# Optimization experiments

Hardware: AMD Instinct MI355X
Metric: run time of the kernel (lower is better)

## Reference

```python
import jax, jax.numpy as jnp
import numpy as np

B, T, I, H, L = 256, 256, 16, 512, 4


def _lstm_layer(x, w_ih, w_hh, b_ih, b_hh):
    """One PyTorch-style LSTM layer. x: [B,T,Din] -> [B,T,H]. Gate order i,f,g,o."""
    Bn = x.shape[0]
    Hn = w_hh.shape[1]
    # precompute input contribution for all timesteps (both biases folded in)
    xg = jnp.einsum('btd,gd->btg', x, w_ih) + b_ih + b_hh  # [B,T,4H]

    def step(carry, xg_t):
        h, c = carry
        g = xg_t + h @ w_hh.T  # [B,4H]
        i, f, gg, o = jnp.split(g, 4, axis=-1)
        i = jax.nn.sigmoid(i)
        f = jax.nn.sigmoid(f)
        gg = jnp.tanh(gg)
        o = jax.nn.sigmoid(o)
        c = f * c + i * gg
        h = o * jnp.tanh(c)
        return (h, c), h

    init = (jnp.zeros((Bn, Hn), x.dtype), jnp.zeros((Bn, Hn), x.dtype))
    _, hs = jax.lax.scan(step, init, jnp.swapaxes(xg, 0, 1))  # hs: [T,B,H]
    return jnp.swapaxes(hs, 0, 1)


def setup_inputs() -> dict:
    key = jax.random.key(0)
    ks = jax.random.split(key, 12)
    s = 1.0 / np.sqrt(H)  # PyTorch LSTM init scale
    inp = {
        'x': jax.random.normal(ks[0], (B, T, I), jnp.float32),
        'w_ih0': jax.random.normal(ks[1], (4 * H, I), jnp.float32) * s,
        'w_hh0': jax.random.normal(ks[2], (4 * H, H), jnp.float32) * s,
        'b_ih0': jax.random.normal(ks[3], (4 * H,), jnp.float32) * s,
        'b_hh0': jax.random.normal(ks[4], (4 * H,), jnp.float32) * s,
        'w_ih_r': jax.random.normal(ks[5], (L - 1, 4 * H, H), jnp.float32) * s,
        'w_hh_r': jax.random.normal(ks[6], (L - 1, 4 * H, H), jnp.float32) * s,
        'b_ih_r': jax.random.normal(ks[7], (L - 1, 4 * H), jnp.float32) * s,
        'b_hh_r': jax.random.normal(ks[8], (L - 1, 4 * H), jnp.float32) * s,
        'fc_w': jax.random.normal(ks[9], (1, H), jnp.float32) * s,
        'fc_b': jax.random.normal(ks[10], (1,), jnp.float32) * s,
    }
    return inp


def reference(x, w_ih0, w_hh0, b_ih0, b_hh0, w_ih_r, w_hh_r, b_ih_r, b_hh_r, fc_w, fc_b):
    # 4-layer LSTM (eval mode: inter-layer dropout is identity)
    h = _lstm_layer(x, w_ih0, w_hh0, b_ih0, b_hh0)
    for l in range(L - 1):
        h = _lstm_layer(h, w_ih_r[l], w_hh_r[l], b_ih_r[l], b_hh_r[l])
    last = h[:, -1, :]  # [B,H]
    return jax.nn.sigmoid(last @ fc_w.T + fc_b)  # [B,1]
```

## Files before the change

kernel.cpp:

```cpp
#include <hip/hip_runtime.h>

#define BB 256
#define TT 256
#define II 16
#define HH 512
#define G4 2048
#define LL 4

typedef float f32x4 __attribute__((ext_vector_type(4)));
typedef _Float16 f16x8 __attribute__((ext_vector_type(8)));
typedef _Float16 f16x4 __attribute__((ext_vector_type(4)));
typedef float f32x4v __attribute__((ext_vector_type(4)));
typedef unsigned int u32x4 __attribute__((ext_vector_type(4)));

#define MFMA16(a, b, c) __builtin_amdgcn_mfma_f32_16x16x32_f16((a), (b), (c), 0, 0, 0)

__device__ _Float16 g_hbuf[(size_t)LL * BB * TT * HH];
__device__ _Float16 g_xbf[(size_t)BB * TT * II];
__device__ _Float16 g_wih0[G4 * II];
__device__ _Float16 g_whh[(size_t)LL * G4 * HH];
__device__ _Float16 g_wihr[(size_t)3 * G4 * HH];
__device__ float    g_bias[LL * G4];
__device__ unsigned g_cnt[32 * 64];

__device__ __forceinline__ void st_cv(void* p, unsigned v) {
  asm volatile("global_store_dword %0, %1, off sc0 sc1" : : "v"(p), "v"(v) : "memory");
}
__device__ __forceinline__ float fsig(float x) { return 1.f / (1.f + __expf(-x)); }
__device__ __forceinline__ float ftanh(float x) { return 1.f - 2.f / (__expf(2.f * x) + 1.f); }

__device__ __forceinline__ unsigned ld_ctr(const unsigned* p) {
  return __hip_atomic_load(p, __ATOMIC_RELAXED, __HIP_MEMORY_SCOPE_AGENT);
}

__device__ __forceinline__ f16x8 ldsA(const _Float16* base, int mt, int kt, int lane) {
  int row = mt * 16 + (lane & 15);
  int off = (row << 10) + (kt << 6) + ((lane >> 4) << 4);
  off ^= (lane & 15) << 4;
  return *(const f16x8*)((const char*)base + off);
}

__device__ __forceinline__ void cv4(_Float16* d, const float* s, size_t n4, size_t tid, size_t stride) {
  for (size_t i = tid; i < n4; i += stride) {
    f32x4v v = ((const f32x4v*)s)[i];
    ((f16x4*)d)[i] = __builtin_convertvector(v, f16x4);
  }
}

__global__ void prep_kernel(const float* __restrict__ x, const float* __restrict__ wih0,
                            const float* __restrict__ whh0, const float* __restrict__ bih0,
                            const float* __restrict__ bhh0, const float* __restrict__ wihr,
                            const float* __restrict__ whhr, const float* __restrict__ bihr,
                            const float* __restrict__ bhhr) {
  size_t tid = (size_t)blockIdx.x * blockDim.x + threadIdx.x;
  size_t stride = (size_t)gridDim.x * blockDim.x;
  cv4(g_xbf, x, (size_t)BB * TT * II / 4, tid, stride);
  cv4(g_wih0, wih0, (size_t)G4 * II / 4, tid, stride);
  cv4(g_whh, whh0, (size_t)G4 * HH / 4, tid, stride);
  cv4(g_whh + (size_t)G4 * HH, whhr, (size_t)3 * G4 * HH / 4, tid, stride);
  cv4(g_wihr, wihr, (size_t)3 * G4 * HH / 4, tid, stride);
  for (size_t i = tid; i < G4; i += stride) g_bias[i] = bih0[i] + bhh0[i];
  for (size_t i = tid; i < 3 * G4; i += stride) g_bias[G4 + i] = bihr[i] + bhhr[i];
  if (tid < 32) g_cnt[tid * 64] = 0u;
}

__global__ __launch_bounds__(256, 1) void lstm_kernel() {
  const int tid = threadIdx.x;
  const int g = blockIdx.x & 7;
  const int jc = blockIdx.x >> 3;
  const int w = tid >> 6;
  const int lane = tid & 63;
  const int col = lane & 15, kg = lane >> 4;
  const int n0 = w * 512 + jc * 16;

  __shared__ _Float16 xs[32 * 512];
  __shared__ _Float16 hs[32 * 512];
  __shared__ float gbuf[4][32 * 17];

  const int eb = tid >> 3;
  const int ej = (tid & 7) * 2;

  f16x8 wihf[16], whhf[16];
  unsigned* cown = &g_cnt[g * 64];

  if (tid < 64) {
    int row = tid >> 1, half = tid & 1;
    int off = (row << 10) + 32 + (half << 4); off ^= (row & 15) << 4;
    u32x4 z = {0u, 0u, 0u, 0u};
    *(u32x4*)((char*)xs + off) = z;
  }

  for (int l = 0; l < LL; ++l) {
    {
      const _Float16* wb = g_whh + ((size_t)l * G4 + (n0 + col)) * HH + kg * 8;
#pragma unroll
      for (int kt = 0; kt < 16; ++kt) whhf[kt] = *(const f16x8*)(wb + kt * 32);
      if (l == 0) {
        if (kg < 2) wihf[0] = *(const f16x8*)(g_wih0 + (n0 + col) * II + kg * 8);
        else { f16x8 z = {}; wihf[0] = z; }
      } else {
        const _Float16* wi = g_wihr + ((size_t)(l - 1) * G4 + (n0 + col)) * HH + kg * 8;
#pragma unroll
        for (int kt = 0; kt < 16; ++kt) wihf[kt] = *(const f16x8*)(wi + kt * 32);
      }
    }
    const float bias = g_bias[l * G4 + n0 + col];
    float c0 = 0.f, c1 = 0.f;

    const _Float16* xsrc = g_hbuf + ((size_t)(l - 1) * BB + 32 * g) * TT * HH;
    _Float16* hdst = g_hbuf + ((size_t)l * BB + 32 * g) * TT * HH;

    u32x4 vx[8], vx0;
    if (l > 0) {
#pragma unroll
      for (int it = 0; it < 8; ++it) {
        int q = tid + it * 256, row = q >> 6, c16 = q & 63;
        vx[it] = *(const u32x4*)((const char*)(xsrc + (size_t)row * TT * HH) + c16 * 16);
      }
    } else if (tid < 64) {
      int row = tid >> 1, half = tid & 1;
      vx0 = *(const u32x4*)(g_xbf + ((size_t)(32 * g + row) * TT) * II + half * 8);
    }

    for (int t = 0; t < TT; ++t) {
      if (l > 0) {
#pragma unroll
        for (int it = 0; it < 8; ++it) {
          int q = tid + it * 256, row = q >> 6, c16 = q & 63;
          int off = (row << 10) + (c16 << 4); off ^= (row & 15) << 4;
          *(u32x4*)((char*)xs + off) = vx[it];
        }
      } else if (tid < 64) {
        int row = tid >> 1, half = tid & 1;
        int off = (row << 10) + (half << 4); off ^= (row & 15) << 4;
        *(u32x4*)((char*)xs + off) = vx0;
      }

      if (t > 0 && tid == 0) {
        unsigned tgt = 32u * (unsigned)(l * TT + t);
        while (ld_ctr(cown) < tgt) {}
      }
      __syncthreads();

      u32x4 vh[8];
      if (t > 0) {
        const _Float16* sh = hdst + (size_t)(t - 1) * HH;
#pragma unroll
        for (int it = 0; it < 8; ++it) {
          int q = tid + it * 256, row = q >> 6, c16 = q & 63;
          vh[it] = *(const u32x4*)((const char*)(sh + (size_t)row * TT * HH) + c16 * 16);
        }
      }

      f32x4 acc0 = {bias, bias, bias, bias}, acc1 = acc0;
      if (l == 0) {
        acc0 = MFMA16(ldsA(xs, 0, 0, lane), wihf[0], acc0);
        acc1 = MFMA16(ldsA(xs, 1, 0, lane), wihf[0], acc1);
      } else {
#pragma unroll
        for (int kt = 0; kt < 16; ++kt) {
          acc0 = MFMA16(ldsA(xs, 0, kt, lane), wihf[kt], acc0);
          acc1 = MFMA16(ldsA(xs, 1, kt, lane), wihf[kt], acc1);
        }
      }

      if (t > 0) {
#pragma unroll
        for (int it = 0; it < 8; ++it) {
          int q = tid + it * 256, row = q >> 6, c16 = q & 63;
          int off = (row << 10) + (c16 << 4); off ^= (row & 15) << 4;
          *(u32x4*)((char*)hs + off) = vh[it];
        }
        __syncthreads();
      }
      if (t + 1 < TT) {
        if (l > 0) {
          const _Float16* sx = xsrc + (size_t)(t + 1) * HH;
#pragma unroll
          for (int it = 0; it < 8; ++it) {
            int q = tid + it * 256, row = q >> 6, c16 = q & 63;
            vx[it] = *(const u32x4*)((const char*)(sx + (size_t)row * TT * HH) + c16 * 16);
          }
        } else if (tid < 64) {
          int row = tid >> 1, half = tid & 1;
          vx0 = *(const u32x4*)(g_xbf + ((size_t)(32 * g + row) * TT + (t + 1)) * II + half * 8);
        }
      }
      if (t > 0) {
#pragma unroll
        for (int kt = 0; kt < 16; ++kt) {
          acc0 = MFMA16(ldsA(hs, 0, kt, lane), whhf[kt], acc0);
          acc1 = MFMA16(ldsA(hs, 1, kt, lane), whhf[kt], acc1);
        }
      }

#pragma unroll
      for (int r = 0; r < 4; ++r) {
        gbuf[w][(kg * 4 + r) * 17 + col] = acc0[r];
        gbuf[w][(16 + kg * 4 + r) * 17 + col] = acc1[r];
      }
      __syncthreads();

      {
        int i0 = eb * 17 + ej;
        float i_0 = fsig(gbuf[0][i0]),  i_1 = fsig(gbuf[0][i0 + 1]);
        float f_0 = fsig(gbuf[1][i0]),  f_1 = fsig(gbuf[1][i0 + 1]);
        float t_0 = ftanh(gbuf[2][i0]), t_1 = ftanh(gbuf[2][i0 + 1]);
        float o_0 = fsig(gbuf[3][i0]),  o_1 = fsig(gbuf[3][i0 + 1]);
        c0 = f_0 * c0 + i_0 * t_0;
        c1 = f_1 * c1 + i_1 * t_1;
        float h0 = o_0 * ftanh(c0), h1 = o_1 * ftanh(c1);
        _Float16 hh0 = (_Float16)h0, hh1 = (_Float16)h1;
        unsigned pv = ((unsigned)__builtin_bit_cast(unsigned short, hh1) << 16) |
                      (unsigned)__builtin_bit_cast(unsigned short, hh0);
        _Float16* dst = hdst + ((size_t)eb * TT + t) * HH + jc * 16 + ej;
        st_cv(dst, pv);
      }

      asm volatile("s_waitcnt vmcnt(0)" ::: "memory");
      __syncthreads();
      if (tid == 0) {
        __hip_atomic_fetch_add(cown, 1u, __ATOMIC_RELAXED, __HIP_MEMORY_SCOPE_AGENT);
      }
    }
  }
}

__global__ void fc_kernel(const float* __restrict__ fcw, const float* __restrict__ fcb,
                          float* __restrict__ out) {
  int b = blockIdx.x, lane = threadIdx.x;
  const _Float16* h = g_hbuf + ((size_t)3 * BB + b) * TT * HH + (size_t)(TT - 1) * HH + lane * 8;
  f16x8 hv = *(const f16x8*)h;
  const float* wp = fcw + lane * 8;
  float s = 0.f;
#pragma unroll
  for (int j = 0; j < 8; ++j) s += (float)hv[j] * wp[j];
#pragma unroll
  for (int off = 32; off; off >>= 1) s += __shfl_down(s, off, 64);
  if (lane == 0) out[b] = 1.f / (1.f + __expf(-(s + fcb[0])));
}

extern "C" void kernel_launch(void* const* d_in, const int* in_sizes, int n_in,
                              void* d_out, int out_size, void* d_ws, size_t ws_size,
                              hipStream_t stream) {
  const float* x    = (const float*)d_in[0];
  const float* wih0 = (const float*)d_in[1];
  const float* whh0 = (const float*)d_in[2];
  const float* bih0 = (const float*)d_in[3];
  const float* bhh0 = (const float*)d_in[4];
  const float* wihr = (const float*)d_in[5];
  const float* whhr = (const float*)d_in[6];
  const float* bihr = (const float*)d_in[7];
  const float* bhhr = (const float*)d_in[8];
  const float* fcw  = (const float*)d_in[9];
  const float* fcb  = (const float*)d_in[10];

  prep_kernel<<<dim3(1024), dim3(256), 0, stream>>>(x, wih0, whh0, bih0, bhh0,
                                                    wihr, whhr, bihr, bhhr);
  lstm_kernel<<<dim3(256), dim3(256), 0, stream>>>();
  fc_kernel<<<dim3(256), dim3(64), 0, stream>>>(fcw, fcb, (float*)d_out);
}
```

Before: 4.994 ms.

## Interleave two batch groups per block with per-producer flags and tiled h layout

Halves the grid to 128 blocks, each processing two batch groups in alternation so one group's sync wait can overlap the other's compute. Replaces the shared atomic counter per group with per-producer flag words polled by 32 threads. Changes the hidden-state buffer to a tiled [layer][group][t][jc][row][16] layout so that each block writes a contiguous 1KB chunk with dwordx4 stores and reads contiguous 16KB blobs. The cost is serialized work for two groups per block on fewer CUs, plus more barriers.

```diff
diff --git a/kernel.cpp b/kernel.cpp
--- a/kernel.cpp
+++ b/kernel.cpp
@@ -15,23 +15,28 @@
 
 #define MFMA16(a, b, c) __builtin_amdgcn_mfma_f32_16x16x32_f16((a), (b), (c), 0, 0, 0)
 
-__device__ _Float16 g_hbuf[(size_t)LL * BB * TT * HH];
+__device__ _Float16 g_hx[(size_t)LL * 8 * TT * 32 * 32 * 16];
 __device__ _Float16 g_xbf[(size_t)BB * TT * II];
 __device__ _Float16 g_wih0[G4 * II];
 __device__ _Float16 g_whh[(size_t)LL * G4 * HH];
 __device__ _Float16 g_wihr[(size_t)3 * G4 * HH];
 __device__ float    g_bias[LL * G4];
-__device__ unsigned g_cnt[32 * 64];
-
-__device__ __forceinline__ void st_cv(void* p, unsigned v) {
+__device__ unsigned g_flag[256 * 16];
+
+__device__ __forceinline__ unsigned ld_cv32(const unsigned* p) {
+  unsigned r;
+  asm volatile("global_load_dword %0, %1, off sc0 sc1\n\ts_waitcnt vmcnt(0)"
+               : "=v"(r) : "v"(p) : "memory");
+  return r;
+}
+__device__ __forceinline__ void st_cv32(unsigned* p, unsigned v) {
   asm volatile("global_store_dword %0, %1, off sc0 sc1" : : "v"(p), "v"(v) : "memory");
+}
+__device__ __forceinline__ void st_cv16(void* p, u32x4 v) {
+  asm volatile("global_store_dwordx4 %0, %1, off sc0 sc1" : : "v"(p), "v"(v) : "memory");
 }
 __device__ __forceinline__ float fsig(float x) { return 1.f / (1.f + __expf(-x)); }
 __device__ __forceinline__ float ftanh(float x) { return 1.f - 2.f / (__expf(2.f * x) + 1.f); }
-
-__device__ __forceinline__ unsigned ld_ctr(const unsigned* p) {
-  return __hip_atomic_load(p, __ATOMIC_RELAXED, __HIP_MEMORY_SCOPE_AGENT);
-}
 
 __device__ __forceinline__ f16x8 ldsA(const _Float16* base, int mt, int kt, int lane) {
   int row = mt * 16 + (lane & 15);
@@ -61,13 +66,13 @@
   cv4(g_wihr, wihr, (size_t)3 * G4 * HH / 4, tid, stride);
   for (size_t i = tid; i < G4; i += stride) g_bias[i] = bih0[i] + bhh0[i];
   for (size_t i = tid; i < 3 * G4; i += stride) g_bias[G4 + i] = bihr[i] + bhhr[i];
-  if (tid < 32) g_cnt[tid * 64] = 0u;
+  for (size_t i = tid; i < 256; i += stride) st_cv32(&g_flag[i * 16], 0u);
 }
 
 __global__ __launch_bounds__(256, 1) void lstm_kernel() {
   const int tid = threadIdx.x;
-  const int g = blockIdx.x & 7;
-  const int jc = blockIdx.x >> 3;
+  const int jc = blockIdx.x >> 2;
+  const int gA = blockIdx.x & 3;
   const int w = tid >> 6;
   const int lane = tid & 63;
   const int col = lane & 15, kg = lane >> 4;
@@ -76,18 +81,28 @@
   __shared__ _Float16 xs[32 * 512];
   __shared__ _Float16 hs[32 * 512];
   __shared__ float gbuf[4][32 * 17];
+  __shared__ unsigned hout[32][8];
 
   const int eb = tid >> 3;
-  const int ej = (tid & 7) * 2;
+  const int ej2 = tid & 7;
 
   f16x8 wihf[16], whhf[16];
-  unsigned* cown = &g_cnt[g * 64];
+  u32x4 vx[2][8], vx0[2];
+  float c0[2], c1[2];
+  const int gArr[2] = {gA, gA + 4};
 
   if (tid < 64) {
-    int row = tid >> 1, half = tid & 1;
-    int off = (row << 10) + 32 + (half << 4); off ^= (row & 15) << 4;
+    int row = tid >> 1, part = tid & 1;
+    int off = (row << 10) + 32 + (part << 4); off ^= (row & 15) << 4;
     u32x4 z = {0u, 0u, 0u, 0u};
     *(u32x4*)((char*)xs + off) = z;
+  }
+#pragma unroll
+  for (int sg = 0; sg < 2; ++sg) {
+    if (tid < 64) {
+      int row = tid >> 1, part = tid & 1;
+      vx0[sg] = *(const u32x4*)(g_xbf + ((size_t)(32 * gArr[sg] + row) * TT) * II + part * 8);
+    }
   }
 
   for (int l = 0; l < LL; ++l) {
@@ -105,122 +120,119 @@
       }
     }
     const float bias = g_bias[l * G4 + n0 + col];
-    float c0 = 0.f, c1 = 0.f;
-
-    const _Float16* xsrc = g_hbuf + ((size_t)(l - 1) * BB + 32 * g) * TT * HH;
-    _Float16* hdst = g_hbuf + ((size_t)l * BB + 32 * g) * TT * HH;
-
-    u32x4 vx[8], vx0;
-    if (l > 0) {
-#pragma unroll
-      for (int it = 0; it < 8; ++it) {
-        int q = tid + it * 256, row = q >> 6, c16 = q & 63;
-        vx[it] = *(const u32x4*)((const char*)(xsrc + (size_t)row * TT * HH) + c16 * 16);
-      }
-    } else if (tid < 64) {
-      int row = tid >> 1, half = tid & 1;
-      vx0 = *(const u32x4*)(g_xbf + ((size_t)(32 * g + row) * TT) * II + half * 8);
-    }
+#pragma unroll
+    for (int sg = 0; sg < 2; ++sg) { c0[sg] = 0.f; c1[sg] = 0.f; }
 
     for (int t = 0; t < TT; ++t) {
-      if (l > 0) {
-#pragma unroll
-        for (int it = 0; it < 8; ++it) {
-          int q = tid + it * 256, row = q >> 6, c16 = q & 63;
-          int off = (row << 10) + (c16 << 4); off ^= (row & 15) << 4;
-          *(u32x4*)((char*)xs + off) = vx[it];
-        }
-      } else if (tid < 64) {
-        int row = tid >> 1, half = tid & 1;
-        int off = (row << 10) + (half << 4); off ^= (row & 15) << 4;
-        *(u32x4*)((char*)xs + off) = vx0;
-      }
-
-      if (t > 0 && tid == 0) {
-        unsigned tgt = 32u * (unsigned)(l * TT + t);
-        while (ld_ctr(cown) < tgt) {}
-      }
-      __syncthreads();
-
-      u32x4 vh[8];
-      if (t > 0) {
-        const _Float16* sh = hdst + (size_t)(t - 1) * HH;
-#pragma unroll
-        for (int it = 0; it < 8; ++it) {
-          int q = tid + it * 256, row = q >> 6, c16 = q & 63;
-          vh[it] = *(const u32x4*)((const char*)(sh + (size_t)row * TT * HH) + c16 * 16);
-        }
-      }
-
-      f32x4 acc0 = {bias, bias, bias, bias}, acc1 = acc0;
-      if (l == 0) {
-        acc0 = MFMA16(ldsA(xs, 0, 0, lane), wihf[0], acc0);
-        acc1 = MFMA16(ldsA(xs, 1, 0, lane), wihf[0], acc1);
-      } else {
-#pragma unroll
-        for (int kt = 0; kt < 16; ++kt) {
-          acc0 = MFMA16(ldsA(xs, 0, kt, lane), wihf[kt], acc0);
-          acc1 = MFMA16(ldsA(xs, 1, kt, lane), wihf[kt], acc1);
-        }
-      }
-
-      if (t > 0) {
-#pragma unroll
-        for (int it = 0; it < 8; ++it) {
-          int q = tid + it * 256, row = q >> 6, c16 = q & 63;
-          int off = (row << 10) + (c16 << 4); off ^= (row & 15) << 4;
-          *(u32x4*)((char*)hs + off) = vh[it];
-        }
-        __syncthreads();
-      }
-      if (t + 1 < TT) {
+#pragma unroll
+      for (int sg = 0; sg < 2; ++sg) {
+        const int g = gArr[sg];
+        const size_t blobL = ((size_t)l * 8 + g) * TT;
+
+        const unsigned tgt = (unsigned)(l * TT + t);
+        if (tgt && tid < 64) {
+          const unsigned* fp = &g_flag[(g * 32 + (tid & 31)) * 16];
+          while (ld_cv32(fp) < tgt) {}
+        }
+        __syncthreads();
+
+        if (t == 0 && l > 0) {
+          const char* xb = (const char*)(g_hx + (((size_t)(l - 1) * 8 + g) * TT) * 16384);
+#pragma unroll
+          for (int it = 0; it < 8; ++it)
+            vx[sg][it] = *(const u32x4*)(xb + tid * 16 + it * 4096);
+        }
+        u32x4 vh[8];
+        if (t > 0) {
+          const char* hb = (const char*)(g_hx + (blobL + (t - 1)) * 16384);
+#pragma unroll
+          for (int it = 0; it < 8; ++it)
+            vh[it] = *(const u32x4*)(hb + tid * 16 + it * 4096);
+        }
         if (l > 0) {
-          const _Float16* sx = xsrc + (size_t)(t + 1) * HH;
 #pragma unroll
           for (int it = 0; it < 8; ++it) {
-            int q = tid + it * 256, row = q >> 6, c16 = q & 63;
-            vx[it] = *(const u32x4*)((const char*)(sx + (size_t)row * TT * HH) + c16 * 16);
+            int jcs = (tid >> 6) + it * 4, row = (tid >> 1) & 31, p = tid & 1;
+            int off = (row << 10) + jcs * 32 + (p << 4); off ^= (row & 15) << 4;
+            *(u32x4*)((char*)xs + off) = vx[sg][it];
           }
         } else if (tid < 64) {
-          int row = tid >> 1, half = tid & 1;
-          vx0 = *(const u32x4*)(g_xbf + ((size_t)(32 * g + row) * TT + (t + 1)) * II + half * 8);
-        }
-      }
-      if (t > 0) {
-#pragma unroll
-        for (int kt = 0; kt < 16; ++kt) {
-          acc0 = MFMA16(ldsA(hs, 0, kt, lane), whhf[kt], acc0);
-          acc1 = MFMA16(ldsA(hs, 1, kt, lane), whhf[kt], acc1);
-        }
-      }
-
-#pragma unroll
-      for (int r = 0; r < 4; ++r) {
-        gbuf[w][(kg * 4 + r) * 17 + col] = acc0[r];
-        gbuf[w][(16 + kg * 4 + r) * 17 + col] = acc1[r];
-      }
-      __syncthreads();
-
-      {
-        int i0 = eb * 17 + ej;
-        float i_0 = fsig(gbuf[0][i0]),  i_1 = fsig(gbuf[0][i0 + 1]);
-        float f_0 = fsig(gbuf[1][i0]),  f_1 = fsig(gbuf[1][i0 + 1]);
-        float t_0 = ftanh(gbuf[2][i0]), t_1 = ftanh(gbuf[2][i0 + 1]);
-        float o_0 = fsig(gbuf[3][i0]),  o_1 = fsig(gbuf[3][i0 + 1]);
-        c0 = f_0 * c0 + i_0 * t_0;
-        c1 = f_1 * c1 + i_1 * t_1;
-        float h0 = o_0 * ftanh(c0), h1 = o_1 * ftanh(c1);
-        _Float16 hh0 = (_Float16)h0, hh1 = (_Float16)h1;
-        unsigned pv = ((unsigned)__builtin_bit_cast(unsigned short, hh1) << 16) |
-                      (unsigned)__builtin_bit_cast(unsigned short, hh0);
-        _Float16* dst = hdst + ((size_t)eb * TT + t) * HH + jc * 16 + ej;
-        st_cv(dst, pv);
-      }
-
-      asm volatile("s_waitcnt vmcnt(0)" ::: "memory");
-      __syncthreads();
-      if (tid == 0) {
-        __hip_atomic_fetch_add(cown, 1u, __ATOMIC_RELAXED, __HIP_MEMORY_SCOPE_AGENT);
+          int row = tid >> 1, part = tid & 1;
+          int off = (row << 10) + (part << 4); off ^= (row & 15) << 4;
+          *(u32x4*)((char*)xs + off) = vx0[sg];
+        }
+        __syncthreads();
+
+        f32x4 a0 = {bias, bias, bias, bias}, a1 = a0;
+        if (l == 0) {
+          a0 = MFMA16(ldsA(xs, 0, 0, lane), wihf[0], a0);
+          a1 = MFMA16(ldsA(xs, 1, 0, lane), wihf[0], a1);
+        } else {
+#pragma unroll
+          for (int kt = 0; kt < 16; ++kt) {
+            a0 = MFMA16(ldsA(xs, 0, kt, lane), wihf[kt], a0);
+            a1 = MFMA16(ldsA(xs, 1, kt, lane), wihf[kt], a1);
+          }
+        }
+
+        if (t > 0) {
+#pragma unroll
+          for (int it = 0; it < 8; ++it) {
+            int jcs = (tid >> 6) + it * 4, row = (tid >> 1) & 31, p = tid & 1;
+            int off = (row << 10) + jcs * 32 + (p << 4); off ^= (row & 15) << 4;
+            *(u32x4*)((char*)hs + off) = vh[it];
+          }
+          __syncthreads();
+        }
+        if (t + 1 < TT) {
+          if (l > 0) {
+            const char* xb = (const char*)(g_hx + (((size_t)(l - 1) * 8 + g) * TT + (t + 1)) * 16384);
+#pragma unroll
+            for (int it = 0; it < 8; ++it)
+              vx[sg][it] = *(const u32x4*)(xb + tid * 16 + it * 4096);
+          } else if (tid < 64) {
+            int row = tid >> 1, part = tid & 1;
+            vx0[sg] = *(const u32x4*)(g_xbf + ((size_t)(32 * g + row) * TT + (t + 1)) * II + part * 8);
+          }
+        }
+        if (t > 0) {
+#pragma unroll
+          for (int kt = 0; kt < 16; ++kt) {
+            a0 = MFMA16(ldsA(hs, 0, kt, lane), whhf[kt], a0);
+            a1 = MFMA16(ldsA(hs, 1, kt, lane), whhf[kt], a1);
+          }
+        }
+
+#pragma unroll
+        for (int r = 0; r < 4; ++r) {
+          gbuf[w][(kg * 4 + r) * 17 + col] = a0[r];
+          gbuf[w][(16 + kg * 4 + r) * 17 + col] = a1[r];
+        }
+        __syncthreads();
+
+        {
+          int i0 = eb * 17 + ej2 * 2;
+          float i_0 = fsig(gbuf[0][i0]),  i_1 = fsig(gbuf[0][i0 + 1]);
+          float f_0 = fsig(gbuf[1][i0]),  f_1 = fsig(gbuf[1][i0 + 1]);
+          float t_0 = ftanh(gbuf[2][i0]), t_1 = ftanh(gbuf[2][i0 + 1]);
+          float o_0 = fsig(gbuf[3][i0]),  o_1 = fsig(gbuf[3][i0 + 1]);
+          c0[sg] = f_0 * c0[sg] + i_0 * t_0;
+          c1[sg] = f_1 * c1[sg] + i_1 * t_1;
+          float h0 = o_0 * ftanh(c0[sg]), h1 = o_1 * ftanh(c1[sg]);
+          _Float16 hh0 = (_Float16)h0, hh1 = (_Float16)h1;
+          hout[eb][ej2] = ((unsigned)__builtin_bit_cast(unsigned short, hh1) << 16) |
+                          (unsigned)__builtin_bit_cast(unsigned short, hh0);
+        }
+        __syncthreads();
+
+        if (tid < 64) {
+          int row = tid >> 1, part = tid & 1;
+          u32x4 v = *(const u32x4*)&hout[row][part * 4];
+          _Float16* dst = g_hx + ((blobL + t) * 32 + jc) * 512 + row * 16 + part * 8;
+          st_cv16(dst, v);
+          asm volatile("s_waitcnt vmcnt(0)" ::: "memory");
+          if (tid == 0) st_cv32(&g_flag[(g * 32 + jc) * 16], (unsigned)(l * TT + t + 1));
+        }
       }
     }
   }
@@ -229,7 +241,9 @@
 __global__ void fc_kernel(const float* __restrict__ fcw, const float* __restrict__ fcb,
                           float* __restrict__ out) {
   int b = blockIdx.x, lane = threadIdx.x;
-  const _Float16* h = g_hbuf + ((size_t)3 * BB + b) * TT * HH + (size_t)(TT - 1) * HH + lane * 8;
+  int g = b >> 5, row = b & 31;
+  int jcs = lane >> 1, part = lane & 1;
+  const _Float16* h = g_hx + ((((size_t)3 * 8 + g) * TT + (TT - 1)) * 32 + jcs) * 512 + row * 16 + part * 8;
   f16x8 hv = *(const f16x8*)h;
   const float* wp = fcw + lane * 8;
   float s = 0.f;
@@ -257,6 +271,6 @@
 
   prep_kernel<<<dim3(1024), dim3(256), 0, stream>>>(x, wih0, whh0, bih0, bhh0,
                                                     wihr, whhr, bihr, bhhr);
-  lstm_kernel<<<dim3(256), dim3(256), 0, stream>>>();
+  lstm_kernel<<<dim3(128), dim3(256), 0, stream>>>();
   fc_kernel<<<dim3(256), dim3(64), 0, stream>>>(fcw, fcb, (float*)d_out);
 }
```

After: 8.175 ms. +63.7%, slower.

## Replace counter barrier with poison-sentinel polling on hidden-state data

Applied to the files above, without the earlier changes.

Drops the per-group atomic counter and its spin-wait, along with the end-of-step vmcnt wait, syncthreads and atomic increment. Instead the prep kernel fills the hidden-state buffer with an all-ones poison pattern, and consumers re-load (cache-bypassing) until no poison word remains. The goal is to remove a full round-trip of barrier signalling per timestep so data arrival itself is the synchronisation. In exchange every launch must poison the whole hidden buffer. It also relies on 0xFFFF never being a real fp16 output (it is a NaN pattern) and on the ordering of the 4-byte stores.

```diff
diff --git a/kernel.cpp b/kernel.cpp
--- a/kernel.cpp
+++ b/kernel.cpp
@@ -6,6 +6,7 @@
 #define HH 512
 #define G4 2048
 #define LL 4
+#define POISON 0xFFFFFFFFu
 
 typedef float f32x4 __attribute__((ext_vector_type(4)));
 typedef _Float16 f16x8 __attribute__((ext_vector_type(8)));
@@ -21,16 +22,29 @@
 __device__ _Float16 g_whh[(size_t)LL * G4 * HH];
 __device__ _Float16 g_wihr[(size_t)3 * G4 * HH];
 __device__ float    g_bias[LL * G4];
-__device__ unsigned g_cnt[32 * 64];
-
+
+__device__ __forceinline__ u32x4 ld_cv(const void* p) {
+  u32x4 r;
+  asm volatile("global_load_dwordx4 %0, %1, off sc0 sc1" : "=v"(r) : "v"(p) : "memory");
+  return r;
+}
+__device__ __forceinline__ u32x4 ld_nc(const void* p) {
+  u32x4 r;
+  asm volatile("global_load_dwordx4 %0, %1, off" : "=v"(r) : "v"(p) : "memory");
+  return r;
+}
 __device__ __forceinline__ void st_cv(void* p, unsigned v) {
   asm volatile("global_store_dword %0, %1, off sc0 sc1" : : "v"(p), "v"(v) : "memory");
 }
+#define WAITV0() asm volatile("s_waitcnt vmcnt(0)" ::: "memory")
+#define WAITV1() asm volatile("s_waitcnt vmcnt(1)" ::: "memory")
+
 __device__ __forceinline__ float fsig(float x) { return 1.f / (1.f + __expf(-x)); }
 __device__ __forceinline__ float ftanh(float x) { return 1.f - 2.f / (__expf(2.f * x) + 1.f); }
-
-__device__ __forceinline__ unsigned ld_ctr(const unsigned* p) {
-  return __hip_atomic_load(p, __ATOMIC_RELAXED, __HIP_MEMORY_SCOPE_AGENT);
+__device__ __forceinline__ unsigned max4u(u32x4 v) {
+  unsigned a = v[0] > v[1] ? v[0] : v[1];
+  unsigned b = v[2] > v[3] ? v[2] : v[3];
+  return a > b ? a : b;
 }
 
 __device__ __forceinline__ f16x8 ldsA(const _Float16* base, int mt, int kt, int lane) {
@@ -61,7 +75,10 @@
   cv4(g_wihr, wihr, (size_t)3 * G4 * HH / 4, tid, stride);
   for (size_t i = tid; i < G4; i += stride) g_bias[i] = bih0[i] + bhh0[i];
   for (size_t i = tid; i < 3 * G4; i += stride) g_bias[G4 + i] = bihr[i] + bhhr[i];
-  if (tid < 32) g_cnt[tid * 64] = 0u;
+  u32x4 P = {POISON, POISON, POISON, POISON};
+  size_t n16 = (size_t)LL * BB * TT * HH * 2 / 16;
+  u32x4* hb = (u32x4*)g_hbuf;
+  for (size_t i = tid; i < n16; i += stride) hb[i] = P;
 }
 
 __global__ __launch_bounds__(256, 1) void lstm_kernel() {
@@ -81,7 +98,6 @@
   const int ej = (tid & 7) * 2;
 
   f16x8 wihf[16], whhf[16];
-  unsigned* cown = &g_cnt[g * 64];
 
   if (tid < 64) {
     int row = tid >> 1, half = tid & 1;
@@ -115,15 +131,28 @@
 #pragma unroll
       for (int it = 0; it < 8; ++it) {
         int q = tid + it * 256, row = q >> 6, c16 = q & 63;
-        vx[it] = *(const u32x4*)((const char*)(xsrc + (size_t)row * TT * HH) + c16 * 16);
+        vx[it] = ld_nc((const char*)(xsrc + (size_t)row * TT * HH) + c16 * 16);
       }
     } else if (tid < 64) {
       int row = tid >> 1, half = tid & 1;
-      vx0 = *(const u32x4*)(g_xbf + ((size_t)(32 * g + row) * TT) * II + half * 8);
+      vx0 = ld_nc(g_xbf + ((size_t)(32 * g + row) * TT) * II + half * 8);
     }
 
     for (int t = 0; t < TT; ++t) {
+      if (t == 0) WAITV0(); else WAITV1();
       if (l > 0) {
+        while (true) {
+          unsigned mx = 0u;
+#pragma unroll
+          for (int it = 0; it < 8; ++it) { unsigned m = max4u(vx[it]); mx = mx > m ? mx : m; }
+          if (!__any((int)(mx == POISON))) break;
+#pragma unroll
+          for (int it = 0; it < 8; ++it) {
+            int q = tid + it * 256, row = q >> 6, c16 = q & 63;
+            vx[it] = ld_cv((const char*)(xsrc + (size_t)t * HH + (size_t)row * TT * HH) + c16 * 16);
+          }
+          WAITV0();
+        }
 #pragma unroll
         for (int it = 0; it < 8; ++it) {
           int q = tid + it * 256, row = q >> 6, c16 = q & 63;
@@ -136,35 +165,44 @@
         *(u32x4*)((char*)xs + off) = vx0;
       }
 
-      if (t > 0 && tid == 0) {
-        unsigned tgt = 32u * (unsigned)(l * TT + t);
-        while (ld_ctr(cown) < tgt) {}
-      }
-      __syncthreads();
-
       u32x4 vh[8];
       if (t > 0) {
         const _Float16* sh = hdst + (size_t)(t - 1) * HH;
 #pragma unroll
         for (int it = 0; it < 8; ++it) {
           int q = tid + it * 256, row = q >> 6, c16 = q & 63;
-          vh[it] = *(const u32x4*)((const char*)(sh + (size_t)row * TT * HH) + c16 * 16);
-        }
-      }
-
-      f32x4 acc0 = {bias, bias, bias, bias}, acc1 = acc0;
+          vh[it] = ld_cv((const char*)(sh + (size_t)row * TT * HH) + c16 * 16);
+        }
+      }
+      __syncthreads();
+
+      f32x4 a0 = {bias, bias, bias, bias}, a1 = a0;
       if (l == 0) {
-        acc0 = MFMA16(ldsA(xs, 0, 0, lane), wihf[0], acc0);
-        acc1 = MFMA16(ldsA(xs, 1, 0, lane), wihf[0], acc1);
+        a0 = MFMA16(ldsA(xs, 0, 0, lane), wihf[0], a0);
+        a1 = MFMA16(ldsA(xs, 1, 0, lane), wihf[0], a1);
       } else {
 #pragma unroll
         for (int kt = 0; kt < 16; ++kt) {
-          acc0 = MFMA16(ldsA(xs, 0, kt, lane), wihf[kt], acc0);
-          acc1 = MFMA16(ldsA(xs, 1, kt, lane), wihf[kt], acc1);
+          a0 = MFMA16(ldsA(xs, 0, kt, lane), wihf[kt], a0);
+          a1 = MFMA16(ldsA(xs, 1, kt, lane), wihf[kt], a1);
         }
       }
 
       if (t > 0) {
+        WAITV0();
+        while (true) {
+          unsigned mx = 0u;
+#pragma unroll
+          for (int it = 0; it < 8; ++it) { unsigned m = max4u(vh[it]); mx = mx > m ? mx : m; }
+          if (!__any((int)(mx == POISON))) break;
+          const _Float16* sh = hdst + (size_t)(t - 1) * HH;
+#pragma unroll
+          for (int it = 0; it < 8; ++it) {
+            int q = tid + it * 256, row = q >> 6, c16 = q & 63;
+            vh[it] = ld_cv((const char*)(sh + (size_t)row * TT * HH) + c16 * 16);
+          }
+          WAITV0();
+        }
 #pragma unroll
         for (int it = 0; it < 8; ++it) {
           int q = tid + it * 256, row = q >> 6, c16 = q & 63;
@@ -173,31 +211,33 @@
         }
         __syncthreads();
       }
+
       if (t + 1 < TT) {
         if (l > 0) {
           const _Float16* sx = xsrc + (size_t)(t + 1) * HH;
 #pragma unroll
           for (int it = 0; it < 8; ++it) {
             int q = tid + it * 256, row = q >> 6, c16 = q & 63;
-            vx[it] = *(const u32x4*)((const char*)(sx + (size_t)row * TT * HH) + c16 * 16);
+            vx[it] = ld_nc((const char*)(sx + (size_t)row * TT * HH) + c16 * 16);
           }
         } else if (tid < 64) {
           int row = tid >> 1, half = tid & 1;
-          vx0 = *(const u32x4*)(g_xbf + ((size_t)(32 * g + row) * TT + (t + 1)) * II + half * 8);
-        }
-      }
+          vx0 = ld_nc(g_xbf + ((size_t)(32 * g + row) * TT + (t + 1)) * II + half * 8);
+        }
+      }
+
       if (t > 0) {
 #pragma unroll
         for (int kt = 0; kt < 16; ++kt) {
-          acc0 = MFMA16(ldsA(hs, 0, kt, lane), whhf[kt], acc0);
-          acc1 = MFMA16(ldsA(hs, 1, kt, lane), whhf[kt], acc1);
+          a0 = MFMA16(ldsA(hs, 0, kt, lane), whhf[kt], a0);
+          a1 = MFMA16(ldsA(hs, 1, kt, lane), whhf[kt], a1);
         }
       }
 
 #pragma unroll
       for (int r = 0; r < 4; ++r) {
-        gbuf[w][(kg * 4 + r) * 17 + col] = acc0[r];
-        gbuf[w][(16 + kg * 4 + r) * 17 + col] = acc1[r];
+        gbuf[w][(kg * 4 + r) * 17 + col] = a0[r];
+        gbuf[w][(16 + kg * 4 + r) * 17 + col] = a1[r];
       }
       __syncthreads();
 
@@ -213,14 +253,7 @@
         _Float16 hh0 = (_Float16)h0, hh1 = (_Float16)h1;
         unsigned pv = ((unsigned)__builtin_bit_cast(unsigned short, hh1) << 16) |
                       (unsigned)__builtin_bit_cast(unsigned short, hh0);
-        _Float16* dst = hdst + ((size_t)eb * TT + t) * HH + jc * 16 + ej;
-        st_cv(dst, pv);
-      }
-
-      asm volatile("s_waitcnt vmcnt(0)" ::: "memory");
-      __syncthreads();
-      if (tid == 0) {
-        __hip_atomic_fetch_add(cown, 1u, __ATOMIC_RELAXED, __HIP_MEMORY_SCOPE_AGENT);
+        st_cv(hdst + ((size_t)eb * TT + t) * HH + jc * 16 + ej, pv);
       }
     }
   }
```

Result: faster. 4.090 ms (-18.1%).
